# Performance work log

Hardware: AMD Instinct MI355X
Metric: run time of the kernel (lower is better)

## Reference

```python
import jax, jax.numpy as jnp
import numpy as np

EPS = 1e-5

def _conv(x, w, pad, groups=1):
    return jax.lax.conv_general_dilated(
        x, w, window_strides=(1, 1), padding=[(pad, pad), (pad, pad)],
        dimension_numbers=('NCHW', 'OIHW', 'NCHW'), feature_group_count=groups)

def _bn(x, g, b, m, v):
    # inference batch-norm, per-channel
    s = g * jax.lax.rsqrt(v + EPS)
    return x * s[None, :, None, None] + (b - m * s)[None, :, None, None]

def setup_inputs() -> dict:
    key = jax.random.key(0)
    ks = jax.random.split(key, 20)
    B, C, H, W = 32, 128, 64, 64
    cs = C // 2  # c_split = 64
    d = {
        'x': jax.random.normal(ks[0], (B, C, H, W), jnp.float32),
        'weights': jax.random.uniform(ks[1], (B, 2), jnp.float32),
        'indices': jax.random.randint(ks[2], (B, 2), 0, 4, jnp.int32),
        # expert 0: Conv(cs -> C, k=3, p=1) + BN + SiLU
        'e0_w': jax.random.normal(ks[3], (C, cs, 3, 3), jnp.float32) * 0.05,
        'e0_g': jax.random.uniform(ks[4], (C,), jnp.float32, 0.5, 1.5),
        'e0_b': jax.random.normal(ks[5], (C,), jnp.float32) * 0.1,
        'e0_m': jax.random.normal(ks[6], (C,), jnp.float32) * 0.1,
        'e0_v': jax.random.uniform(ks[7], (C,), jnp.float32, 0.5, 1.5),
        # expert 1: depthwise 5x5 (cs, groups=cs) -> 1x1 (cs -> C) -> BN -> SiLU
        'e1_dw': jax.random.normal(ks[8], (cs, 1, 5, 5), jnp.float32) * 0.05,
        'e1_pw': jax.random.normal(ks[9], (C, cs, 1, 1), jnp.float32) * 0.05,
        'e1_g': jax.random.uniform(ks[10], (C,), jnp.float32, 0.5, 1.5),
        'e1_b': jax.random.normal(ks[11], (C,), jnp.float32) * 0.1,
        'e1_m': jax.random.normal(ks[12], (C,), jnp.float32) * 0.1,
        'e1_v': jax.random.uniform(ks[13], (C,), jnp.float32, 0.5, 1.5),
        # expert 2: GhostConv(C -> C): cv1 = Conv(C, C//2, 3), cv2 = Conv(C//2, C//2, 5, groups=C//2)
        'e2a_w': jax.random.normal(ks[14], (cs, C, 3, 3), jnp.float32) * 0.05,
        'e2a_g': jax.random.uniform(ks[15], (cs,), jnp.float32, 0.5, 1.5),
        'e2a_b': jax.random.normal(ks[16], (cs,), jnp.float32) * 0.1,
        'e2a_m': jax.random.normal(ks[17], (cs,), jnp.float32) * 0.1,
        'e2a_v': jax.random.uniform(ks[18], (cs,), jnp.float32, 0.5, 1.5),
        'e2b_w': jax.random.normal(ks[19], (cs, 1, 5, 5), jnp.float32) * 0.05,
    }
    ks2 = jax.random.split(jax.random.key(1), 4)
    d['e2b_g'] = jax.random.uniform(ks2[0], (cs,), jnp.float32, 0.5, 1.5)
    d['e2b_b'] = jax.random.normal(ks2[1], (cs,), jnp.float32) * 0.1
    d['e2b_m'] = jax.random.normal(ks2[2], (cs,), jnp.float32) * 0.1
    d['e2b_v'] = jax.random.uniform(ks2[3], (cs,), jnp.float32, 0.5, 1.5)
    return d

def _forward(x, weights, indices,
             e0_w, e0_g, e0_b, e0_m, e0_v,
             e1_dw, e1_pw, e1_g, e1_b, e1_m, e1_v,
             e2a_w, e2a_g, e2a_b, e2a_m, e2a_v,
             e2b_w, e2b_g, e2b_b, e2b_m, e2b_v):
    C = x.shape[1]
    cs = C // 2
    x_rgb, x_ir = x[:, :cs], x[:, cs:]
    # expert outputs computed densely over the whole batch, masked combine below
    e0 = jax.nn.silu(_bn(_conv(x_rgb, e0_w, pad=1), e0_g, e0_b, e0_m, e0_v))
    e1 = jax.nn.silu(_bn(_conv(_conv(x_ir, e1_dw, pad=2, groups=cs), e1_pw, pad=0),
                         e1_g, e1_b, e1_m, e1_v))
    g1 = jax.nn.silu(_bn(_conv(x, e2a_w, pad=1), e2a_g, e2a_b, e2a_m, e2a_v))
    g2 = jax.nn.silu(_bn(_conv(g1, e2b_w, pad=2, groups=cs), e2b_g, e2b_b, e2b_m, e2b_v))
    e2 = jnp.concatenate([g1, g2], axis=1)
    out = jnp.zeros_like(x)
    K = indices.shape[1]
    for k in range(K):  # small fixed top-k loop
        idx = indices[:, k][:, None, None, None]          # [B,1,1,1]
        w = weights[:, k][:, None, None, None]            # [B,1,1,1]
        out = out + jnp.where(idx == 0, e0 * w, 0.0)
        out = out + jnp.where(idx == 1, e1 * w, 0.0)
        out = out + jnp.where(idx == 2, e2 * w, 0.0)
        out = out + jnp.where(idx == 3, x * 0.1, 0.0)
    return out

def reference(x, weights, indices,
              e0_w, e0_g, e0_b, e0_m, e0_v,
              e1_dw, e1_pw, e1_g, e1_b, e1_m, e1_v,
              e2a_w, e2a_g, e2a_b, e2a_m, e2a_v,
              e2b_w, e2b_g, e2b_b, e2b_m, e2b_v):
    return _forward(x, weights, indices,
                    e0_w, e0_g, e0_b, e0_m, e0_v,
                    e1_dw, e1_pw, e1_g, e1_b, e1_m, e1_v,
                    e2a_w, e2a_g, e2a_b, e2a_m, e2a_v,
                    e2b_w, e2b_g, e2b_b, e2b_m, e2b_v)
```

## Files before the change

### kernel.cpp

```cpp
#include <hip/hip_runtime.h>

#define B_  32
#define C_  128
#define CS  64
#define H_  64
#define W_  64
#define HW  (H_*W_)

typedef __attribute__((ext_vector_type(8))) short bf16x8_t;
typedef __attribute__((ext_vector_type(4))) float f32x4_t;
typedef unsigned short u16;
typedef unsigned int   u32;

__device__ __forceinline__ float silu_f(float v) { return v / (1.f + __expf(-v)); }

__device__ __forceinline__ u16 f2bf(float f) {
    u32 u = __float_as_uint(f);
    u = (u + 0x7FFFu + ((u >> 16) & 1u)) >> 16;
    return (u16)u;
}
__device__ __forceinline__ float bf2f(u16 u) {
    return __uint_as_float(((u32)u) << 16);
}
__device__ __forceinline__ u32 pack2(float a, float b) {
    return (u32)f2bf(a) | ((u32)f2bf(b) << 16);
}

__device__ __forceinline__ void get_coeffs(const float* __restrict__ wts,
                                           const int* __restrict__ idxs, int b,
                                           float& c0, float& c1, float& c2, float& cid) {
    int   i0 = idxs[b*2+0], i1 = idxs[b*2+1];
    float w0 = wts[b*2+0],  w1 = wts[b*2+1];
    c0  = (i0==0?w0:0.f)   + (i1==0?w1:0.f);
    c1  = (i0==1?w0:0.f)   + (i1==1?w1:0.f);
    c2  = (i0==2?w0:0.f)   + (i1==2?w1:0.f);
    cid = (i0==3?0.1f:0.f) + (i1==3?0.1f:0.f);
}

__global__ __launch_bounds__(256) void k_prep(
    const float* __restrict__ e0w, const float* __restrict__ e2aw, const float* __restrict__ e1pw,
    u16* __restrict__ Wt0f, u16* __restrict__ Wt2f, u16* __restrict__ Wt1f)
{
    const int i0 = blockIdx.x*256 + threadIdx.x, stride = gridDim.x*256;
    for (int i = i0; i < 73728; i += stride) {
        int j = i&7, lane = (i>>3)&63, cog = (i>>9)&7, kc = (i>>12)&1, tap = i>>13;
        int co = cog*16 + (lane&15), ci = kc*32 + (lane>>4)*8 + j;
        Wt0f[i] = f2bf(e0w[(size_t)(co*64 + ci)*9 + tap]);
    }
    for (int i = i0; i < 73728; i += stride) {
        int j = i&7, lane = (i>>3)&63, cog = (i>>9)&3, kc = (i>>11)&3, tap = i>>13;
        int co = cog*16 + (lane&15), ci = kc*32 + (lane>>4)*8 + j;
        Wt2f[i] = f2bf(e2aw[(size_t)(co*128 + ci)*9 + tap]);
    }
    for (int i = i0; i < 8192; i += stride) {
        int j = i&7, lane = (i>>3)&63, cog = (i>>9)&7, kc = (i>>12)&1;
        int co = cog*16 + (lane&15), ci = kc*32 + (lane>>4)*8 + j;
        Wt1f[i] = f2bf(e1pw[(size_t)co*64 + ci]);
    }
}

__global__ __launch_bounds__(256) void k_to_nhwc(
    const float* __restrict__ x, const float* __restrict__ wts, const int* __restrict__ idxs,
    u16* __restrict__ xhA, u16* __restrict__ xhB)
{
    const int b = blockIdx.y, h = blockIdx.x, t = threadIdx.x;
    float c0, c1, c2, cid;
    get_coeffs(wts, idxs, b, c0, c1, c2, cid);
    if (c0 == 0.f && c2 == 0.f) return;
    const int np = (c2 != 0.f) ? 2 : 1;
    const int chmax = np*64;

    __shared__ float ld[128*66];
    for (int i = t; i < chmax*16; i += 256) {
        int ch = i >> 4, q = i & 15;
        float4 v = *(const float4*)(x + ((size_t)(b*C_+ch))*HW + h*64 + q*4);
        float* p = &ld[ch*66 + q*4];
        p[0] = v.x; p[1] = v.y; p[2] = v.z; p[3] = v.w;
    }
    __syncthreads();

    const int px = t >> 2, sub = t & 3;
    const size_t base64 = ((size_t)(b*66 + h+1)*66 + (px+1))*64;
    for (int c = sub; c < chmax/8; c += 4) {
        uint4 v;
        u32 w[4];
        #pragma unroll
        for (int k = 0; k < 4; ++k)
            w[k] = pack2(ld[(c*8 + 2*k)*66 + px], ld[(c*8 + 2*k + 1)*66 + px]);
        v.x = w[0]; v.y = w[1]; v.z = w[2]; v.w = w[3];
        u16* dst = (c < 8) ? (xhA + base64 + c*8) : (xhB + base64 + (c-8)*8);
        *(uint4*)dst = v;
    }
    for (int i = t; i < 16*np; i += 256) {
        int pl = i >> 4, j = i & 15;
        int col = (j >> 3)*65, cg = j & 7;
        u16* ph = pl ? xhB : xhA;
        uint4 z; z.x = z.y = z.z = z.w = 0u;
        *(uint4*)(ph + ((size_t)(b*66 + h+1)*66 + col)*64 + cg*8) = z;
    }
    if (h == 0 || h == 63) {
        int r = (h == 0) ? 0 : 65;
        for (int i = t; i < 66*8*np; i += 256) {
            int pl = i / (66*8), j = i % (66*8);
            int col = j >> 3, cg = j & 7;
            u16* ph = pl ? xhB : xhA;
            uint4 z; z.x = z.y = z.z = z.w = 0u;
            *(uint4*)(ph + ((size_t)(b*66 + r)*66 + (size_t)col)*64 + cg*8) = z;
        }
    }
}

template<int NCF, int NPF, int TK, int COUT>
__device__ __forceinline__ void conv_pass(
    const char* lin, const u16* __restrict__ wb, int koff,
    int rbase, int pxbase, int l15, int kg,
    f32x4_t (&acc)[NCF][NPF])
{
    bf16x8_t A0[NCF], A1[NCF], A2[NCF];

    auto issueA = [&](int i, bf16x8_t (&dst)[NCF]) {
        const int tap = i >> 1, kcl = i & 1;
        const u16* wt = wb + (size_t)((tap*TK + koff + kcl)*(COUT/16))*512;
        #pragma unroll
        for (int cf = 0; cf < NCF; ++cf)
            asm volatile("global_load_dwordx4 %0, %1, off"
                         : "=v"(dst[cf]) : "v"(wt + ((size_t)cf << 9)));
    };
    auto ldsB = [&](int i, int pf) -> bf16x8_t {
        const int tap = i >> 1, kcl = i & 1;
        const int dh = tap / 3, dwp = tap % 3;
        const int p = (rbase + dh)*66 + pxbase + pf*16 + l15 + dwp;
        u32 a = (u32)p*128 + (u32)kcl*64 + (u32)kg*16;
        a ^= ((u32)(p & 7)) << 4;
        return *(const bf16x8_t*)(lin + a);
    };

    issueA(0, A0);
    issueA(1, A1);
    #pragma unroll
    for (int i = 0; i < 18; ++i) {
        if (i + 2 < 18) {
            const int s = (i + 2) % 3;
            if (s == 0)      issueA(i + 2, A0);
            else if (s == 1) issueA(i + 2, A1);
            else             issueA(i + 2, A2);
        }
        if (i < 16)       asm volatile("s_waitcnt vmcnt(8)" ::: "memory");
        else if (i == 16) asm volatile("s_waitcnt vmcnt(4)" ::: "memory");
        else              asm volatile("s_waitcnt vmcnt(0)" ::: "memory");
        __builtin_amdgcn_sched_barrier(0);
        bf16x8_t* ac = (i % 3 == 0) ? A0 : ((i % 3 == 1) ? A1 : A2);
        #pragma unroll
        for (int pf = 0; pf < NPF; ++pf) {
            bf16x8_t bfr = ldsB(i, pf);
            #pragma unroll
            for (int cf = 0; cf < NCF; ++cf)
                acc[cf][pf] = __builtin_amdgcn_mfma_f32_16x16x32_bf16(ac[cf], bfr, acc[cf][pf], 0, 0, 0);
        }
    }
}

__global__ __launch_bounds__(256, 3) void k_conv(
    const u16* __restrict__ xhA, const u16* __restrict__ xhB, const float* __restrict__ x,
    const float* __restrict__ wts, const int* __restrict__ idxs,
    const u16* __restrict__ Wt0f, const u16* __restrict__ Wt2f,
    const float* __restrict__ e0g, const float* __restrict__ e0b,
    const float* __restrict__ e0m, const float* __restrict__ e0v,
    const float* __restrict__ e2ag, const float* __restrict__ e2ab,
    const float* __restrict__ e2am, const float* __restrict__ e2av,
    float* __restrict__ out, u16* __restrict__ g1)
{
    __shared__ char lin[33792];
    const int b = blockIdx.y, orow0 = blockIdx.x*2, t = threadIdx.x;
    float c0, c1, c2, cid;
    get_coeffs(wts, idxs, b, c0, c1, c2, cid);

    const int lane = t & 63, l15 = lane & 15, kg = lane >> 4, wv = t >> 6;
    const size_t src0 = ((size_t)(b*66 + orow0))*66*64;

    auto stage = [&](const u16* src) {
        const char* sp = (const char*)src;
        for (int d = t*16; d < 33792; d += 4096) {
            u32 s = (u32)d ^ ((((u32)d >> 7) & 7u) << 4);
            *(uint4*)(lin + d) = *(const uint4*)(sp + s);
        }
    };

    if (blockIdx.z == 0) {
        if (c0 == 0.f) {
            for (int i = t; i < 4096; i += 256) {
                int ch = i >> 5, q = i & 31;
                size_t o = ((size_t)(b*C_+ch))*HW + (size_t)orow0*64 + q*4;
                float4 ov;
                if (cid != 0.f) {
                    float4 xv = *(const float4*)(x + o);
                    ov.x = cid*xv.x; ov.y = cid*xv.y; ov.z = cid*xv.z; ov.w = cid*xv.w;
                } else { ov.x = ov.y = ov.z = ov.w = 0.f; }
                *(float4*)(out + o) = ov;
            }
            return;
        }
        stage(xhA + src0);
        __syncthreads();

        const int cw = wv >> 1, rw = wv & 1;
        const int cobase = cw*64;
        f32x4_t acc[4][4];
        #pragma unroll
        for (int cf = 0; cf < 4; ++cf)
            #pragma unroll
            for (int pf = 0; pf < 4; ++pf)
                acc[cf][pf] = (f32x4_t){0.f, 0.f, 0.f, 0.f};

        const u16* wb = Wt0f + (size_t)(cobase >> 4)*512 + (size_t)lane*8;
        conv_pass<4, 4, 2, 128>(lin, wb, 0, rw, 0, l15, kg, acc);

        #pragma unroll
        for (int cf = 0; cf < 4; ++cf) {
            float sarr[4], tarr[4];
            #pragma unroll
            for (int r = 0; r < 4; ++r) {
                int co = cobase + cf*16 + kg*4 + r;
                float s = e0g[co] * rsqrtf(e0v[co] + 1e-5f);
                sarr[r] = s; tarr[r] = e0b[co] - e0m[co]*s;
            }
            #pragma unroll
            for (int pf = 0; pf < 4; ++pf) {
                size_t rowoff = (size_t)(orow0 + rw)*64 + pf*16 + l15;
                #pragma unroll
                for (int r = 0; r < 4; ++r) {
                    int co = cobase + cf*16 + kg*4 + r;
                    float v = silu_f(acc[cf][pf][r]*sarr[r] + tarr[r]);
                    size_t o = ((size_t)(b*C_+co))*HW + rowoff;
                    float idv = (cid != 0.f) ? cid*x[o] : 0.f;
                    out[o] = c0*v + idv;
                }
            }
        }
    } else {
        if (c2 == 0.f) return;

        const int rw = wv >> 1, pw = wv & 1;
        const int pxbase = pw*32;
        f32x4_t acc[4][2];
        #pragma unroll
        for (int cf = 0; cf < 4; ++cf)
            #pragma unroll
            for (int pf = 0; pf < 2; ++pf)
                acc[cf][pf] = (f32x4_t){0.f, 0.f, 0.f, 0.f};

        const u16* wb = Wt2f + (size_t)lane*8;

        stage(xhA + src0);
        __syncthreads();
        conv_pass<4, 2, 4, 64>(lin, wb, 0, rw, pxbase, l15, kg, acc);
        __syncthreads();
        stage(xhB + src0);
        __syncthreads();
        conv_pass<4, 2, 4, 64>(lin, wb, 2, rw, pxbase, l15, kg, acc);

        #pragma unroll
        for (int cf = 0; cf < 4; ++cf) {
            float sarr[4], tarr[4];
            #pragma unroll
            for (int r = 0; r < 4; ++r) {
                int co = cf*16 + kg*4 + r;
                float s = e2ag[co] * rsqrtf(e2av[co] + 1e-5f);
                sarr[r] = s; tarr[r] = e2ab[co] - e2am[co]*s;
            }
            #pragma unroll
            for (int pf = 0; pf < 2; ++pf) {
                size_t rowoff = (size_t)(orow0 + rw)*64 + pxbase + pf*16 + l15;
                #pragma unroll
                for (int r = 0; r < 4; ++r) {
                    int co = cf*16 + kg*4 + r;
                    float v = silu_f(acc[cf][pf][r]*sarr[r] + tarr[r]);
                    g1[((size_t)(b*CS+co))*HW + rowoff] = f2bf(v);
                }
            }
        }
    }
}

__global__ __launch_bounds__(256) void k_e1(
    const float* __restrict__ x, const float* __restrict__ wts, const int* __restrict__ idxs,
    const float* __restrict__ dww, const u16* __restrict__ Wt1f,
    const float* __restrict__ gg, const float* __restrict__ bb,
    const float* __restrict__ mm, const float* __restrict__ vv,
    float* __restrict__ out)
{
    const int b = blockIdx.y, band = blockIdx.x, t = threadIdx.x;
    const int orow0 = band*2;

    float c0, c1, c2, cid;
    get_coeffs(wts, idxs, b, c0, c1, c2, cid);
    if (c1 == 0.f) return;

    __shared__ u16  lin[6*64*70];
    __shared__ u16  lout[128*72];
    __shared__ float wl[64*26];

    for (int i = t; i < 64*25; i += 256) wl[(i/25)*26 + (i%25)] = dww[i];
    for (int i = t; i < 6*64*16; i += 256) {
        int q = i & 15, ch = (i >> 4) & 63, r = i >> 10;
        int hh = orow0 - 2 + r;
        u32 w0 = 0u, w1 = 0u;
        if (hh >= 0 && hh < H_) {
            float4 v = *(const float4*)(x + ((size_t)(b*C_ + CS + ch))*HW + hh*64 + q*4);
            w0 = pack2(v.x, v.y); w1 = pack2(v.z, v.w);
        }
        u32* dst = (u32*)&lin[(r*64 + ch)*70 + 2 + q*4];
        dst[0] = w0; dst[1] = w1;
    }
    for (int i = t; i < 6*64; i += 256) {
        int ch = i & 63, r = i >> 6;
        *(u32*)&lin[(r*64 + ch)*70]      = 0u;
        u32* e = (u32*)&lin[(r*64 + ch)*70 + 66];
        e[0] = 0u; e[1] = 0u;
    }
    __syncthreads();

    const int lane = t & 63, chl = lane & 15, cs = lane >> 4;
    const int wv = t >> 6, outrow = wv & 1, chhalf = wv >> 1;

    #pragma unroll
    for (int chi = 0; chi < 2; ++chi) {
        const int ch = chhalf*32 + chl + chi*16;
        const float* wch = &wl[ch*26];
        float accp[16];
        #pragma unroll
        for (int p = 0; p < 16; ++p) accp[p] = 0.f;
        #pragma unroll
        for (int kh = 0; kh < 5; ++kh) {
            const u16* src = &lin[((outrow + kh)*64 + ch)*70 + cs*16];
            float rb[20];
            #pragma unroll
            for (int k = 0; k < 10; ++k) {
                u32 u = *(const u32*)(src + 2*k);
                rb[2*k]   = __uint_as_float(u << 16);
                rb[2*k+1] = __uint_as_float(u & 0xFFFF0000u);
            }
            #pragma unroll
            for (int kw = 0; kw < 5; ++kw) {
                float wvv = wch[kh*5 + kw];
                #pragma unroll
                for (int p = 0; p < 16; ++p) accp[p] += rb[p+kw]*wvv;
            }
        }
        const int px0 = outrow*64 + cs*16;
        #pragma unroll
        for (int p = 0; p < 16; ++p) lout[(px0+p)*72 + ch] = f2bf(accp[p]);
    }
    __syncthreads();

    const int l15 = lane & 15, kg = lane >> 4;
    const int cw = wv >> 1, pwv = wv & 1;
    f32x4_t acc[4][4];
    #pragma unroll
    for (int cf = 0; cf < 4; ++cf)
        #pragma unroll
        for (int pf = 0; pf < 4; ++pf)
            acc[cf][pf] = (f32x4_t){0.f, 0.f, 0.f, 0.f};

    #pragma unroll
    for (int kc = 0; kc < 2; ++kc) {
        const u16* wt = Wt1f + (((size_t)(kc*8 + cw*4)) << 9) + lane*8;
        bf16x8_t af[4];
        #pragma unroll
        for (int cf = 0; cf < 4; ++cf) af[cf] = *(const bf16x8_t*)(wt + (cf << 9));
        const int k0 = kc*32 + kg*8;
        #pragma unroll
        for (int pf = 0; pf < 4; ++pf) {
            bf16x8_t bfr = *(const bf16x8_t*)&lout[(pwv*64 + pf*16 + l15)*72 + k0];
            #pragma unroll
            for (int cf = 0; cf < 4; ++cf)
                acc[cf][pf] = __builtin_amdgcn_mfma_f32_16x16x32_bf16(af[cf], bfr, acc[cf][pf], 0, 0, 0);
        }
    }

    #pragma unroll
    for (int cf = 0; cf < 4; ++cf) {
        float sarr[4], tarr[4];
        #pragma unroll
        for (int r = 0; r < 4; ++r) {
            int co = cw*64 + cf*16 + kg*4 + r;
            float s = gg[co] * rsqrtf(vv[co] + 1e-5f);
            sarr[r] = s; tarr[r] = bb[co] - mm[co]*s;
        }
        #pragma unroll
        for (int pf = 0; pf < 4; ++pf) {
            int px = pwv*64 + pf*16 + l15;
            size_t rowoff = (size_t)(orow0 + (px>>6))*64 + (px&63);
            #pragma unroll
            for (int r = 0; r < 4; ++r) {
                int co = cw*64 + cf*16 + kg*4 + r;
                float v = silu_f(acc[cf][pf][r]*sarr[r] + tarr[r]);
                out[((size_t)(b*C_+co))*HW + rowoff] += c1*v;
            }
        }
    }
}

__global__ __launch_bounds__(256) void k_e2b(
    const u16* __restrict__ g1, const float* __restrict__ wts, const int* __restrict__ idxs,
    const float* __restrict__ dww, const float* __restrict__ gg, const float* __restrict__ bb,
    const float* __restrict__ mm, const float* __restrict__ vv, float* __restrict__ out)
{
    const int b = blockIdx.y, band = blockIdx.x, t = threadIdx.x;
    const int orow0 = band*2;

    float c0, c1, c2, cid;
    get_coeffs(wts, idxs, b, c0, c1, c2, cid);
    if (c2 == 0.f) return;

    __shared__ u16  lin[6*64*70];
    __shared__ float wl[64*26];

    for (int i = t; i < 64*25; i += 256) wl[(i/25)*26 + (i%25)] = dww[i];
    for (int i = t; i < 6*64*16; i += 256) {
        int q = i & 15, ch = (i >> 4) & 63, r = i >> 10;
        int hh = orow0 - 2 + r;
        u32 w0 = 0u, w1 = 0u;
        if (hh >= 0 && hh < H_) {
            const u32* src = (const u32*)(g1 + ((size_t)(b*CS+ch))*HW + hh*64 + q*4);
            w0 = src[0]; w1 = src[1];
        }
        u32* dst = (u32*)&lin[(r*64 + ch)*70 + 2 + q*4];
        dst[0] = w0; dst[1] = w1;
    }
    for (int i = t; i < 6*64; i += 256) {
        int ch = i & 63, r = i >> 6;
        *(u32*)&lin[(r*64 + ch)*70] = 0u;
        u32* e = (u32*)&lin[(r*64 + ch)*70 + 66];
        e[0] = 0u; e[1] = 0u;
    }
    __syncthreads();

    for (int i = t; i < 2*64*16; i += 256) {
        int q = i & 15, ch = (i >> 4) & 63, r = i >> 10;
        const u16* src = &lin[((r+2)*64 + ch)*70 + 2 + q*4];
        float* op = out + ((size_t)(b*C_+ch))*HW + (size_t)(orow0+r)*64 + q*4;
        float4 ov = *(float4*)op;
        ov.x += c2*bf2f(src[0]); ov.y += c2*bf2f(src[1]);
        ov.z += c2*bf2f(src[2]); ov.w += c2*bf2f(src[3]);
        *(float4*)op = ov;
    }

    const int lane = t & 63, chl = lane & 15, cs = lane >> 4;
    const int wv = t >> 6, outrow = wv & 1, chhalf = wv >> 1;

    #pragma unroll
    for (int chi = 0; chi < 2; ++chi) {
        const int ch = chhalf*32 + chl + chi*16;
        const float* wch = &wl[ch*26];
        float accp[16];
        #pragma unroll
        for (int p = 0; p < 16; ++p) accp[p] = 0.f;
        #pragma unroll
        for (int kh = 0; kh < 5; ++kh) {
            const u16* src = &lin[((outrow + kh)*64 + ch)*70 + cs*16];
            float rb[20];
            #pragma unroll
            for (int k = 0; k < 10; ++k) {
                u32 u = *(const u32*)(src + 2*k);
                rb[2*k]   = __uint_as_float(u << 16);
                rb[2*k+1] = __uint_as_float(u & 0xFFFF0000u);
            }
            #pragma unroll
            for (int kw = 0; kw < 5; ++kw) {
                float wvv = wch[kh*5 + kw];
                #pragma unroll
                for (int p = 0; p < 16; ++p) accp[p] += rb[p+kw]*wvv;
            }
        }
        float s = gg[ch] * rsqrtf(vv[ch] + 1e-5f);
        float tt = bb[ch] - mm[ch]*s;
        float* op = out + ((size_t)(b*C_ + CS + ch))*HW + (size_t)(orow0+outrow)*64 + cs*16;
        #pragma unroll
        for (int q = 0; q < 4; ++q) {
            float4 ov = *(float4*)(op + q*4);
            ov.x += c2*silu_f(accp[q*4+0]*s + tt);
            ov.y += c2*silu_f(accp[q*4+1]*s + tt);
            ov.z += c2*silu_f(accp[q*4+2]*s + tt);
            ov.w += c2*silu_f(accp[q*4+3]*s + tt);
            *(float4*)(op + q*4) = ov;
        }
    }
}

extern "C" void kernel_launch(void* const* d_in, const int* in_sizes, int n_in,
                              void* d_out, int out_size, void* d_ws, size_t ws_size,
                              hipStream_t stream) {
    const float* x    = (const float*)d_in[0];
    const float* wts  = (const float*)d_in[1];
    const int*   idxs = (const int*)  d_in[2];
    const float* e0w  = (const float*)d_in[3];
    const float* e0g  = (const float*)d_in[4];
    const float* e0b  = (const float*)d_in[5];
    const float* e0m  = (const float*)d_in[6];
    const float* e0v  = (const float*)d_in[7];
    const float* e1dw = (const float*)d_in[8];
    const float* e1pw = (const float*)d_in[9];
    const float* e1g  = (const float*)d_in[10];
    const float* e1b  = (const float*)d_in[11];
    const float* e1m  = (const float*)d_in[12];
    const float* e1v  = (const float*)d_in[13];
    const float* e2aw = (const float*)d_in[14];
    const float* e2ag = (const float*)d_in[15];
    const float* e2ab = (const float*)d_in[16];
    const float* e2am = (const float*)d_in[17];
    const float* e2av = (const float*)d_in[18];
    const float* e2bw = (const float*)d_in[19];
    const float* e2bg = (const float*)d_in[20];
    const float* e2bb = (const float*)d_in[21];
    const float* e2bm = (const float*)d_in[22];
    const float* e2bv = (const float*)d_in[23];

    float* out = (float*)d_out;

    const size_t PLANE = (size_t)32*66*66*64;
    u16* xhA  = (u16*)d_ws;
    u16* xhB  = xhA + PLANE;
    u16* g1   = xhB + PLANE;
    u16* Wt0f = g1 + (size_t)8388608;
    u16* Wt2f = Wt0f + 73728;
    u16* Wt1f = Wt2f + 73728;

    k_prep<<<128, 256, 0, stream>>>(e0w, e2aw, e1pw, Wt0f, Wt2f, Wt1f);
    k_to_nhwc<<<dim3(64, B_), 256, 0, stream>>>(x, wts, idxs, xhA, xhB);
    k_conv<<<dim3(32, B_, 2), 256, 0, stream>>>(
        xhA, xhB, x, wts, idxs, Wt0f, Wt2f,
        e0g, e0b, e0m, e0v, e2ag, e2ab, e2am, e2av, out, g1);
    k_e1<<<dim3(32, B_), 256, 0, stream>>>(
        x, wts, idxs, e1dw, Wt1f, e1g, e1b, e1m, e1v, out);
    k_e2b<<<dim3(32, B_), 256, 0, stream>>>(
        g1, wts, idxs, e2bw, e2bg, e2bb, e2bm, e2bv, out);
}
```

Before: 107.9 us.

## Fuse NCHW-to-NHWC bf16 conversion into conv kernel staging

Removes the separate k_to_nhwc pass that wrote padded bf16 NHWC copies of x to workspace. The conv kernel now reads fp32 NCHW rows of x directly, converts them to bf16 and writes them into the swizzled LDS layout, handling halo zero padding inline. This drops a full write and reread of the padded intermediate and one kernel launch. In exchange each conv block redoes the conversion for its overlapping halo rows, and the fp32 global loads are strided per channel instead of contiguous 16-byte chunks.

```diff
diff --git a/kernel.cpp b/kernel.cpp
--- a/kernel.cpp
+++ b/kernel.cpp
@@ -59,54 +59,35 @@
     }
 }
 
-__global__ __launch_bounds__(256) void k_to_nhwc(
-    const float* __restrict__ x, const float* __restrict__ wts, const int* __restrict__ idxs,
-    u16* __restrict__ xhA, u16* __restrict__ xhB)
+__device__ __forceinline__ void stage_x(
+    const float* __restrict__ xb,
+    char* lin, int orow0, int t)
 {
-    const int b = blockIdx.y, h = blockIdx.x, t = threadIdx.x;
-    float c0, c1, c2, cid;
-    get_coeffs(wts, idxs, b, c0, c1, c2, cid);
-    if (c0 == 0.f && c2 == 0.f) return;
-    const int np = (c2 != 0.f) ? 2 : 1;
-    const int chmax = np*64;
-
-    __shared__ float ld[128*66];
-    for (int i = t; i < chmax*16; i += 256) {
-        int ch = i >> 4, q = i & 15;
-        float4 v = *(const float4*)(x + ((size_t)(b*C_+ch))*HW + h*64 + q*4);
-        float* p = &ld[ch*66 + q*4];
-        p[0] = v.x; p[1] = v.y; p[2] = v.z; p[3] = v.w;
-    }
-    __syncthreads();
-
-    const int px = t >> 2, sub = t & 3;
-    const size_t base64 = ((size_t)(b*66 + h+1)*66 + (px+1))*64;
-    for (int c = sub; c < chmax/8; c += 4) {
-        uint4 v;
-        u32 w[4];
-        #pragma unroll
-        for (int k = 0; k < 4; ++k)
-            w[k] = pack2(ld[(c*8 + 2*k)*66 + px], ld[(c*8 + 2*k + 1)*66 + px]);
-        v.x = w[0]; v.y = w[1]; v.z = w[2]; v.w = w[3];
-        u16* dst = (c < 8) ? (xhA + base64 + c*8) : (xhB + base64 + (c-8)*8);
-        *(uint4*)dst = v;
-    }
-    for (int i = t; i < 16*np; i += 256) {
-        int pl = i >> 4, j = i & 15;
-        int col = (j >> 3)*65, cg = j & 7;
-        u16* ph = pl ? xhB : xhA;
-        uint4 z; z.x = z.y = z.z = z.w = 0u;
-        *(uint4*)(ph + ((size_t)(b*66 + h+1)*66 + col)*64 + cg*8) = z;
-    }
-    if (h == 0 || h == 63) {
-        int r = (h == 0) ? 0 : 65;
-        for (int i = t; i < 66*8*np; i += 256) {
-            int pl = i / (66*8), j = i % (66*8);
-            int col = j >> 3, cg = j & 7;
-            u16* ph = pl ? xhB : xhA;
-            uint4 z; z.x = z.y = z.z = z.w = 0u;
-            *(uint4*)(ph + ((size_t)(b*66 + r)*66 + (size_t)col)*64 + cg*8) = z;
-        }
+    #pragma unroll
+    for (int k = 0; k < 8; ++k) {
+        const int u = t + k*256;
+        const int quad = u & 15, r = (u >> 4) & 3, cp = u >> 6;
+        const int hh = orow0 - 1 + r;
+        float4 v0, v1;
+        if (hh >= 0 && hh < H_) {
+            v0 = *(const float4*)(xb + (size_t)(2*cp)*HW + hh*64 + quad*4);
+            v1 = *(const float4*)(xb + (size_t)(2*cp+1)*HW + hh*64 + quad*4);
+        } else {
+            v0.x = v0.y = v0.z = v0.w = 0.f;
+            v1.x = v1.y = v1.z = v1.w = 0.f;
+        }
+        #pragma unroll
+        for (int j = 0; j < 4; ++j) {
+            const int p = r*66 + quad*4 + j + 1;
+            const u32 a = ((u32)p*128 + (u32)cp*4) ^ (((u32)(p & 7)) << 4);
+            *(u32*)(lin + a) = pack2((&v0.x)[j], (&v1.x)[j]);
+        }
+    }
+    {
+        const int cp = t & 31, side = (t >> 5) & 1, r = t >> 6;
+        const int p = r*66 + side*65;
+        const u32 a = ((u32)p*128 + (u32)cp*4) ^ (((u32)(p & 7)) << 4);
+        *(u32*)(lin + a) = 0u;
     }
 }
 
@@ -161,7 +142,7 @@
 }
 
 __global__ __launch_bounds__(256, 3) void k_conv(
-    const u16* __restrict__ xhA, const u16* __restrict__ xhB, const float* __restrict__ x,
+    const float* __restrict__ x,
     const float* __restrict__ wts, const int* __restrict__ idxs,
     const u16* __restrict__ Wt0f, const u16* __restrict__ Wt2f,
     const float* __restrict__ e0g, const float* __restrict__ e0b,
@@ -176,15 +157,7 @@
     get_coeffs(wts, idxs, b, c0, c1, c2, cid);
 
     const int lane = t & 63, l15 = lane & 15, kg = lane >> 4, wv = t >> 6;
-    const size_t src0 = ((size_t)(b*66 + orow0))*66*64;
-
-    auto stage = [&](const u16* src) {
-        const char* sp = (const char*)src;
-        for (int d = t*16; d < 33792; d += 4096) {
-            u32 s = (u32)d ^ ((((u32)d >> 7) & 7u) << 4);
-            *(uint4*)(lin + d) = *(const uint4*)(sp + s);
-        }
-    };
+    const float* xb = x + (size_t)b*C_*HW;
 
     if (blockIdx.z == 0) {
         if (c0 == 0.f) {
@@ -200,7 +173,7 @@
             }
             return;
         }
-        stage(xhA + src0);
+        stage_x(xb, lin, orow0, t);
         __syncthreads();
 
         const int cw = wv >> 1, rw = wv & 1;
@@ -251,11 +224,11 @@
 
         const u16* wb = Wt2f + (size_t)lane*8;
 
-        stage(xhA + src0);
+        stage_x(xb, lin, orow0, t);
         __syncthreads();
         conv_pass<4, 2, 4, 64>(lin, wb, 0, rw, pxbase, l15, kg, acc);
         __syncthreads();
-        stage(xhB + src0);
+        stage_x(xb + (size_t)CS*HW, lin, orow0, t);
         __syncthreads();
         conv_pass<4, 2, 4, 64>(lin, wb, 2, rw, pxbase, l15, kg, acc);
 
@@ -518,18 +491,14 @@
 
     float* out = (float*)d_out;
 
-    const size_t PLANE = (size_t)32*66*66*64;
-    u16* xhA  = (u16*)d_ws;
-    u16* xhB  = xhA + PLANE;
-    u16* g1   = xhB + PLANE;
+    u16* g1   = (u16*)d_ws;
     u16* Wt0f = g1 + (size_t)8388608;
     u16* Wt2f = Wt0f + 73728;
     u16* Wt1f = Wt2f + 73728;
 
     k_prep<<<128, 256, 0, stream>>>(e0w, e2aw, e1pw, Wt0f, Wt2f, Wt1f);
-    k_to_nhwc<<<dim3(64, B_), 256, 0, stream>>>(x, wts, idxs, xhA, xhB);
     k_conv<<<dim3(32, B_, 2), 256, 0, stream>>>(
-        xhA, xhB, x, wts, idxs, Wt0f, Wt2f,
+        x, wts, idxs, Wt0f, Wt2f,
         e0g, e0b, e0m, e0v, e2ag, e2ab, e2am, e2av, out, g1);
     k_e1<<<dim3(32, B_), 256, 0, stream>>>(
         x, wts, idxs, e1dw, Wt1f, e1g, e1b, e1m, e1v, out);
```

Result: faster. 104.7 us (-3.0%).
